# Performance work log

Hardware: AMD Instinct MI355X
Metric: run time of the kernel (lower is better)

The kernel has to match this reference:

```python
import jax, jax.numpy as jnp
import numpy as np


def setup_inputs() -> dict:
    key = jax.random.key(0)
    ks = jax.random.split(key, 6)
    B, C, D, H, O = 4096, 64, 512, 1024, 1
    z = jax.random.normal(ks[0], (B, D), dtype=jnp.float32)
    company_id = jax.random.randint(ks[1], (B,), 0, C)
    # PyTorch Linear default init ~ U(-1/sqrt(fan_in), 1/sqrt(fan_in)); use scaled normals for simplicity
    W1 = jax.random.normal(ks[2], (C, D, H), dtype=jnp.float32) / np.sqrt(D)
    b1 = jax.random.normal(ks[3], (C, H), dtype=jnp.float32) * 0.01
    W2 = jax.random.normal(ks[4], (C, H, O), dtype=jnp.float32) / np.sqrt(H)
    b2 = jax.random.normal(ks[5], (C, O), dtype=jnp.float32) * 0.01
    return {"z": z, "company_id": company_id, "W1": W1, "b1": b1, "W2": W2, "b2": b2}


def reference(z, company_id, W1, b1, W2, b2):
    # Faithful to original: every company head is applied to the full batch,
    # then the single needed row per sample is gathered (dropout is identity in eval).
    # h: [B, C, H]
    h = jnp.einsum("bd,cdh->bch", z, W1) + b1[None, :, :]
    h = jax.nn.gelu(h, approximate=False)  # nn.GELU default = exact erf GELU
    # all_outputs: [B, C, O]
    all_outputs = jnp.einsum("bch,cho->bco", h, W2) + b2[None, :, :]
    # gather the per-sample company row -> [B, O]
    outputs = jnp.take_along_axis(all_outputs, company_id[:, None, None], axis=1)[:, 0, :]
    return outputs
```

## Files before the change

kernel.cpp:

```cpp
#include <hip/hip_runtime.h>

typedef float f32x16 __attribute__((ext_vector_type(16)));
typedef short s16x8  __attribute__((ext_vector_type(8)));

#define B_SZ 4096
#define C_N  64
#define D_K  512
#define H_N  1024
#define BK   16
#define NT   32
#define ROWS 128
#define ZP_OFF_BYTES 32768
#define ZP_ROWS (B_SZ + 128)

__device__ __forceinline__ short f2bf(float f){
  unsigned u = __float_as_uint(f);
  u += 0x7FFFu + ((u >> 16) & 1u);
  return (short)(u >> 16);
}
__device__ __forceinline__ float erf_fast(float x){
  float ax = fabsf(x);
  float t = __builtin_amdgcn_rcpf(1.0f + 0.3275911f * ax);
  float p = t * (0.254829592f + t * (-0.284496736f + t * (1.421413741f +
            t * (-1.453152027f + t * 1.061405429f))));
  float r = 1.0f - p * __expf(-ax * ax);
  return copysignf(r, x);
}
__device__ __forceinline__ float gelu_exact(float x){
  return 0.5f * x * (1.0f + erf_fast(x * 0.70710678118654752f));
}

__global__ void k_prep(const int* __restrict__ cid, const float* __restrict__ b2,
                       int* __restrict__ offsets, int* __restrict__ bucket,
                       float* __restrict__ out){
  __shared__ int hist[C_N];
  const int tid = threadIdx.x;
  if (tid < C_N) hist[tid] = 0;
  __syncthreads();
  for (int i = tid; i < B_SZ; i += 1024) atomicAdd(&hist[cid[i]], 1);
  __syncthreads();
  if (tid < 64){
    int v = hist[tid];
    int x = v;
    #pragma unroll
    for (int d = 1; d < 64; d <<= 1){
      int y = __shfl_up(x, d, 64);
      if (tid >= d) x += y;
    }
    offsets[tid] = x - v;
    if (tid == 63) offsets[64] = x;
    hist[tid] = x - v;
  }
  __syncthreads();
  for (int i = tid; i < B_SZ; i += 1024){
    int c = cid[i];
    int p = atomicAdd(&hist[c], 1);
    bucket[p] = i;
    out[i] = b2[c];
  }
}

__global__ void k_zpack(const float* __restrict__ z, const int* __restrict__ bucket,
                        short* __restrict__ zp){
  int u = blockIdx.x * 256 + threadIdx.x;
  int slot = u >> 6;
  int k0 = (u & 63) * 8;
  const float* src = z + (size_t)bucket[slot] * D_K + k0;
  float4 a = *(const float4*)src;
  float4 b = *(const float4*)(src + 4);
  s16x8 v;
  v[0]=f2bf(a.x); v[1]=f2bf(a.y); v[2]=f2bf(a.z); v[3]=f2bf(a.w);
  v[4]=f2bf(b.x); v[5]=f2bf(b.y); v[6]=f2bf(b.z); v[7]=f2bf(b.w);
  *(s16x8*)(zp + ((size_t)slot << 9) + k0) = v;
}

__global__ __launch_bounds__(256, 2) void k_main(
    const short* __restrict__ zp, const float* __restrict__ W1,
    const float* __restrict__ b1, const float* __restrict__ W2,
    const int* __restrict__ offsets, const int* __restrict__ bucket,
    float* __restrict__ out)
{
  __shared__ float B_lds[4][BK * 128];
  __shared__ char  A_lds[4][4096];
  __shared__ float partial[ROWS];

  const int bid = blockIdx.x;
  const int c = bid & 63, hs = bid >> 6;
  const int off_c = offsets[c];
  const int n_c = offsets[c + 1] - off_c;
  if (n_c == 0) return;

  const int tid  = threadIdx.x;
  const int lane = tid & 63, wave = tid >> 6;
  const int l31 = lane & 31, lhi = lane >> 5;
  const int hcol = hs * 128 + wave * 32 + l31;
  const float b1v = b1[c * H_N + hcol];
  const float w2v = W2[c * H_N + hcol];
  const float* Wpanel = W1 + (size_t)c * D_K * H_N + hs * 128;

  const int r0 = tid >> 5;
  const int hc = (tid & 31) * 4;
  const int arow = tid >> 1;
  const int akh  = (tid & 1) * 8;

  if (tid < ROWS) partial[tid] = 0.0f;

  for (int rb = 0; rb < n_c; rb += ROWS){
    const short* zrow = zp + ((size_t)(off_c + rb + arow) << 9) + akh;

    auto stage = [&](int t){
      const int s = t & 3;
      const float* bsrc = Wpanel + (size_t)(t * BK + r0) * H_N + hc;
      __builtin_amdgcn_global_load_lds(
        (const __attribute__((address_space(1))) void*)bsrc,
        (__attribute__((address_space(3))) void*)(&B_lds[s][r0 * 128 + hc]), 16, 0, 0);
      __builtin_amdgcn_global_load_lds(
        (const __attribute__((address_space(1))) void*)(bsrc + 8 * H_N),
        (__attribute__((address_space(3))) void*)(&B_lds[s][(r0 + 8) * 128 + hc]), 16, 0, 0);
      __builtin_amdgcn_global_load_lds(
        (const __attribute__((address_space(1))) void*)(zrow + t * BK),
        (__attribute__((address_space(3))) void*)(&A_lds[s][tid * 16]), 16, 0, 0);
    };

    stage(0); stage(1); stage(2);

    f32x16 acc[4];
    acc[0] = 0; acc[1] = 0; acc[2] = 0; acc[3] = 0;

    for (int t = 0; t < NT; ++t){
      if (t + 3 < NT) stage(t + 3);
      if      (t <  NT - 3) asm volatile("s_waitcnt vmcnt(9)" ::: "memory");
      else if (t == NT - 3) asm volatile("s_waitcnt vmcnt(6)" ::: "memory");
      else if (t == NT - 2) asm volatile("s_waitcnt vmcnt(3)" ::: "memory");
      else                  asm volatile("s_waitcnt vmcnt(0)" ::: "memory");
      __builtin_amdgcn_s_barrier();

      const int s = t & 3;
      const float* Bt = &B_lds[s][0];
      s16x8 bf;
      #pragma unroll
      for (int e = 0; e < 8; ++e)
        bf[e] = f2bf(Bt[(lhi * 8 + e) * 128 + wave * 32 + l31]);
      const s16x8* At = (const s16x8*)&A_lds[s][0];
      #pragma unroll
      for (int m = 0; m < 4; ++m){
        s16x8 af = At[(m * 32 + l31) * 2 + lhi];
        acc[m] = __builtin_amdgcn_mfma_f32_32x32x16_bf16(af, bf, acc[m], 0, 0, 0);
      }
      __builtin_amdgcn_s_barrier();
    }

    #pragma unroll
    for (int m = 0; m < 4; ++m){
      #pragma unroll
      for (int r = 0; r < 16; ++r){
        int r_loc = m * 32 + (r & 3) + 8 * (r >> 2) + 4 * lhi;
        float v = gelu_exact(acc[m][r] + b1v) * w2v;
        v += __shfl_xor(v, 1, 64);
        v += __shfl_xor(v, 2, 64);
        v += __shfl_xor(v, 4, 64);
        v += __shfl_xor(v, 8, 64);
        v += __shfl_xor(v, 16, 64);
        if (l31 == 0 && rb + r_loc < n_c)
          atomicAdd(&partial[r_loc], v);
      }
    }
    __syncthreads();
    if (tid < ROWS){
      int g = rb + tid;
      if (g < n_c)
        atomicAdd(&out[bucket[off_c + g]], partial[tid]);
      partial[tid] = 0.0f;
    }
  }
}

extern "C" void kernel_launch(void* const* d_in, const int* in_sizes, int n_in,
                              void* d_out, int out_size, void* d_ws, size_t ws_size,
                              hipStream_t stream){
  const float* z  = (const float*)d_in[0];
  const int*   cid= (const int*)  d_in[1];
  const float* W1 = (const float*)d_in[2];
  const float* b1 = (const float*)d_in[3];
  const float* W2 = (const float*)d_in[4];
  const float* b2 = (const float*)d_in[5];
  float* out = (float*)d_out;

  int*   ws      = (int*)d_ws;
  int*   offsets = ws;
  int*   bucket  = ws + 128;
  short* zp      = (short*)((char*)d_ws + ZP_OFF_BYTES);

  k_prep <<<1, 1024, 0, stream>>>(cid, b2, offsets, bucket, out);
  k_zpack<<<1024, 256, 0, stream>>>(z, bucket, zp);
  k_main <<<C_N * 8, 256, 0, stream>>>(zp, W1, b1, W2, offsets, bucket, out);
}
```

Before: 52.71 us.

## Restructure prep/pack kernels, reorder A LDS layout, drop per-iteration trailing barrier

Splits preprocessing into a count/scan kernel and a pack kernel. The pack kernel scatters rows with a global atomic cursor and converts z to bf16 in the same pass, which removes the dependency on a fully built bucket array. In the main kernel, the A tile LDS layout is reordered so each lane reads a contiguous s16x8. Staging is issued after the barrier, and the trailing per-iteration barrier is removed; an extra sync is added after each row block. The atomic-cursor scatter makes bucket order nondeterministic, so the float atomic accumulation order can vary between runs.

```diff
diff --git a/kernel.cpp b/kernel.cpp
--- a/kernel.cpp
+++ b/kernel.cpp
@@ -30,9 +30,8 @@
   return 0.5f * x * (1.0f + erf_fast(x * 0.70710678118654752f));
 }
 
-__global__ void k_prep(const int* __restrict__ cid, const float* __restrict__ b2,
-                       int* __restrict__ offsets, int* __restrict__ bucket,
-                       float* __restrict__ out){
+__global__ void k_cs(const int* __restrict__ cid, int* __restrict__ offsets,
+                     int* __restrict__ cursor){
   __shared__ int hist[C_N];
   const int tid = threadIdx.x;
   if (tid < C_N) hist[tid] = 0;
@@ -48,30 +47,39 @@
       if (tid >= d) x += y;
     }
     offsets[tid] = x - v;
+    cursor[tid]  = x - v;
     if (tid == 63) offsets[64] = x;
-    hist[tid] = x - v;
-  }
-  __syncthreads();
-  for (int i = tid; i < B_SZ; i += 1024){
+  }
+}
+
+__global__ void k_pack(const int* __restrict__ cid, const float* __restrict__ z,
+                       const float* __restrict__ b2, int* __restrict__ cursor,
+                       int* __restrict__ bucket, short* __restrict__ zp,
+                       float* __restrict__ out){
+  __shared__ int pos_s[64];
+  const int tid = threadIdx.x;
+  const int base = blockIdx.x * 64;
+  if (tid < 64){
+    int i = base + tid;
     int c = cid[i];
-    int p = atomicAdd(&hist[c], 1);
+    int p = atomicAdd(&cursor[c], 1);
+    pos_s[tid] = p;
     bucket[p] = i;
     out[i] = b2[c];
   }
-}
-
-__global__ void k_zpack(const float* __restrict__ z, const int* __restrict__ bucket,
-                        short* __restrict__ zp){
-  int u = blockIdx.x * 256 + threadIdx.x;
-  int slot = u >> 6;
-  int k0 = (u & 63) * 8;
-  const float* src = z + (size_t)bucket[slot] * D_K + k0;
-  float4 a = *(const float4*)src;
-  float4 b = *(const float4*)(src + 4);
-  s16x8 v;
-  v[0]=f2bf(a.x); v[1]=f2bf(a.y); v[2]=f2bf(a.z); v[3]=f2bf(a.w);
-  v[4]=f2bf(b.x); v[5]=f2bf(b.y); v[6]=f2bf(b.z); v[7]=f2bf(b.w);
-  *(s16x8*)(zp + ((size_t)slot << 9) + k0) = v;
+  __syncthreads();
+  #pragma unroll
+  for (int j = 0; j < 16; ++j){
+    int u = tid + 256 * j;
+    int s = u >> 6, oct = u & 63;
+    const float* src = z + (size_t)(base + s) * D_K + oct * 8;
+    float4 a = *(const float4*)src;
+    float4 b = *(const float4*)(src + 4);
+    s16x8 v;
+    v[0]=f2bf(a.x); v[1]=f2bf(a.y); v[2]=f2bf(a.z); v[3]=f2bf(a.w);
+    v[4]=f2bf(b.x); v[5]=f2bf(b.y); v[6]=f2bf(b.z); v[7]=f2bf(b.w);
+    *(s16x8*)(zp + ((size_t)pos_s[s] << 9) + oct * 8) = v;
+  }
 }
 
 __global__ __launch_bounds__(256, 2) void k_main(
@@ -81,7 +89,7 @@
     float* __restrict__ out)
 {
   __shared__ float B_lds[4][BK * 128];
-  __shared__ char  A_lds[4][4096];
+  __shared__ s16x8 A_lds[4][256];
   __shared__ float partial[ROWS];
 
   const int bid = blockIdx.x;
@@ -100,8 +108,8 @@
 
   const int r0 = tid >> 5;
   const int hc = (tid & 31) * 4;
-  const int arow = tid >> 1;
-  const int akh  = (tid & 1) * 8;
+  const int arow = ((tid >> 6) << 5) | (tid & 31);
+  const int akh  = ((tid >> 5) & 1) * 8;
 
   if (tid < ROWS) partial[tid] = 0.0f;
 
@@ -119,7 +127,7 @@
         (__attribute__((address_space(3))) void*)(&B_lds[s][(r0 + 8) * 128 + hc]), 16, 0, 0);
       __builtin_amdgcn_global_load_lds(
         (const __attribute__((address_space(1))) void*)(zrow + t * BK),
-        (__attribute__((address_space(3))) void*)(&A_lds[s][tid * 16]), 16, 0, 0);
+        (__attribute__((address_space(3))) void*)(&A_lds[s][tid]), 16, 0, 0);
     };
 
     stage(0); stage(1); stage(2);
@@ -128,12 +136,11 @@
     acc[0] = 0; acc[1] = 0; acc[2] = 0; acc[3] = 0;
 
     for (int t = 0; t < NT; ++t){
-      if (t + 3 < NT) stage(t + 3);
-      if      (t <  NT - 3) asm volatile("s_waitcnt vmcnt(9)" ::: "memory");
-      else if (t == NT - 3) asm volatile("s_waitcnt vmcnt(6)" ::: "memory");
+      if      (t <  NT - 2) asm volatile("s_waitcnt vmcnt(6)" ::: "memory");
       else if (t == NT - 2) asm volatile("s_waitcnt vmcnt(3)" ::: "memory");
       else                  asm volatile("s_waitcnt vmcnt(0)" ::: "memory");
       __builtin_amdgcn_s_barrier();
+      if (t + 3 < NT) stage(t + 3);
 
       const int s = t & 3;
       const float* Bt = &B_lds[s][0];
@@ -141,13 +148,12 @@
       #pragma unroll
       for (int e = 0; e < 8; ++e)
         bf[e] = f2bf(Bt[(lhi * 8 + e) * 128 + wave * 32 + l31]);
-      const s16x8* At = (const s16x8*)&A_lds[s][0];
+      const s16x8* At = &A_lds[s][0];
       #pragma unroll
       for (int m = 0; m < 4; ++m){
-        s16x8 af = At[(m * 32 + l31) * 2 + lhi];
+        s16x8 af = At[m * 64 + lane];
         acc[m] = __builtin_amdgcn_mfma_f32_32x32x16_bf16(af, bf, acc[m], 0, 0, 0);
       }
-      __builtin_amdgcn_s_barrier();
     }
 
     #pragma unroll
@@ -172,6 +178,7 @@
         atomicAdd(&out[bucket[off_c + g]], partial[tid]);
       partial[tid] = 0.0f;
     }
+    __syncthreads();
   }
 }
 
@@ -188,10 +195,11 @@
 
   int*   ws      = (int*)d_ws;
   int*   offsets = ws;
-  int*   bucket  = ws + 128;
+  int*   cursor  = ws + 96;
+  int*   bucket  = ws + 192;
   short* zp      = (short*)((char*)d_ws + ZP_OFF_BYTES);
 
-  k_prep <<<1, 1024, 0, stream>>>(cid, b2, offsets, bucket, out);
-  k_zpack<<<1024, 256, 0, stream>>>(z, bucket, zp);
+  k_cs   <<<1, 1024, 0, stream>>>(cid, offsets, cursor);
+  k_pack <<<64, 256, 0, stream>>>(cid, z, b2, cursor, bucket, zp, out);
   k_main <<<C_N * 8, 256, 0, stream>>>(zp, W1, b1, W2, offsets, bucket, out);
 }
```

Measured after the change: 58.21 us. 10.4% more time.
